# Kernel tuning notes

Hardware: AMD Instinct MI355X
Metric: run time of the kernel (lower is better)

Reference implementation:

```python
import jax, jax.numpy as jnp
import numpy as np

EPS = 1e-8
TAU = 0.2
IOU_THR = 0.5
NEG = -1e9
N, C, H, D_FG, D_CLS = 8192, 1024, 256, 64, 128


def setup_inputs() -> dict:
    key = jax.random.key(0)
    ks = jax.random.split(key, 11)
    def lin(k, fan_in, fan_out):
        return jax.random.normal(k, (fan_in, fan_out), jnp.float32) / np.sqrt(fan_in)
    return {
        "roi_feats": jax.random.normal(ks[0], (N, C), jnp.float32),
        "labels": jax.random.randint(ks[1], (N,), 0, 21, jnp.int32).astype(jnp.int64),
        "ious": jax.random.uniform(ks[2], (N,), jnp.float32),
        "fg_w1": lin(ks[3], C, H), "fg_b1": jnp.zeros((H,), jnp.float32),
        "fg_w2": lin(ks[4], H, D_FG), "fg_b2": jnp.zeros((D_FG,), jnp.float32),
        "cls_w1": lin(ks[5], C, H), "cls_b1": jnp.zeros((H,), jnp.float32),
        "cls_w2": lin(ks[6], H, D_CLS), "cls_b2": jnp.zeros((D_CLS,), jnp.float32),
    }


def _project_normalize(x, w1, b1, w2, b2):
    h = jax.nn.relu(x @ w1 + b1)
    z = h @ w2 + b2
    norm = jnp.maximum(jnp.linalg.norm(z, axis=1, keepdims=True), EPS)
    return z / norm


def _forward(roi_feats, labels, ious, fg_w1, fg_b1, fg_w2, fg_b2, cls_w1, cls_b1, cls_w2, cls_b2):
    n = roi_feats.shape[0]
    z_fg = _project_normalize(roi_feats, fg_w1, fg_b1, fg_w2, fg_b2)
    z_cls = _project_normalize(roi_feats, cls_w1, cls_b1, cls_w2, cls_b2)

    ignore = labels == -1
    fg = (labels > 0) & ~ignore
    iou_weight = jnp.where(ious > IOU_THR, ious, 0.0)
    eye = jnp.eye(n, dtype=bool)

    # ---- fg/bg contrastive (bg_as_negatives_only=True) ----
    sim_fg = (z_fg @ z_fg.T) / TAU                       # [N,N]
    exp_sim = jnp.exp(sim_fg)
    denom = jnp.sum(exp_sim * (~eye).astype(jnp.float32), axis=1)
    pos = (fg & ~ignore)[None, :] & ~eye                 # positives: fg columns, no self
    n_pos = jnp.sum(pos, axis=1)
    numer = jnp.sum(exp_sim * pos.astype(jnp.float32), axis=1)
    # original computes den = denom + EPS then -log((numer+EPS)/(den+EPS))
    loss_i = -jnp.log((numer + EPS) / (denom + 2.0 * EPS))
    valid = (fg & ~ignore) & (n_pos > 0)
    w = iou_weight * valid.astype(jnp.float32)
    loss_fg_bg = jnp.sum(w * loss_i) / (jnp.sum(w) + EPS)

    # ---- class supervised contrastive ----
    sim_cls = (z_cls @ z_cls.T) / TAU
    sim_masked = jnp.where(eye, NEG, sim_cls)
    log_denom = jax.nn.logsumexp(sim_masked, axis=1)     # [N]
    log_p = jnp.where(eye, NEG, sim_cls - log_denom[:, None])
    # pos_mask keeps diagonal (as in original): same label, col not ignore, col label != 0
    posc = (labels[None, :] == labels[:, None]) & (~ignore)[None, :] & (labels[None, :] != 0)
    n_posc = jnp.sum(posc, axis=1).astype(jnp.float32)
    sum_log_p = jnp.sum(log_p * posc.astype(jnp.float32), axis=1)
    valid_c = (fg & ~ignore) & (n_posc > 0) & jnp.isfinite(log_denom)
    Lzi = jnp.where(valid_c, -sum_log_p / (n_posc + EPS), 0.0)
    wc = iou_weight * valid_c.astype(jnp.float32)
    loss_supcon = jnp.sum(wc * Lzi) / (jnp.sum(wc) + EPS)

    return jnp.stack([loss_fg_bg, loss_supcon])


def reference(roi_feats, labels, ious, fg_w1, fg_b1, fg_w2, fg_b2, cls_w1, cls_b1, cls_w2, cls_b2):
    return _forward(roi_feats, labels, ious, fg_w1, fg_b1, fg_w2, fg_b2, cls_w1, cls_b1, cls_w2, cls_b2)
```

## Files before the change

### kernel.cpp

```cpp
#include <hip/hip_runtime.h>


typedef __attribute__((ext_vector_type(8))) short bs8;
typedef __attribute__((ext_vector_type(4))) float f4;

#define MFMA_BF16(a, b, c) __builtin_amdgcn_mfma_f32_16x16x32_bf16((a), (b), (c), 0, 0, 0)

#if defined(__has_builtin)
#if __has_builtin(__builtin_amdgcn_exp2f)
#define EXP2F(x) __builtin_amdgcn_exp2f(x)
#endif
#endif
#ifndef EXP2F
#define EXP2F(x) exp2f(x)
#endif

#define K_LOG2E 7.2134752044448170f

__device__ __forceinline__ unsigned short f2bf(float f) {
  unsigned int u = __float_as_uint(f);
  u = (u + 0x7fffu + ((u >> 16) & 1u)) >> 16;
  return (unsigned short)u;
}
__device__ __forceinline__ float bf2f(unsigned short s) {
  return __uint_as_float(((unsigned int)s) << 16);
}

constexpr size_t O_W1T  = 0;
constexpr size_t O_W2TF = 1048576;
constexpr size_t O_W2TC = 1081344;
constexpr size_t O_H    = 1146880;
constexpr size_t O_ZF   = 9535488;
constexpr size_t O_ZC   = 10584064;
constexpr size_t O_SCLS = 12681216;
constexpr size_t O_ROWD = 12697600;
constexpr size_t O_ROWN = 12730368;
constexpr size_t O_ROWS = 12763136;
constexpr size_t O_SCAL = 12795904;
constexpr size_t O_HIST = 12795920;
constexpr size_t O_NFG  = 12796048;
constexpr int ZERO_WORDS = (int)((O_NFG + 4 - O_SCLS) / 4);

__global__ void __launch_bounds__(256) zero_kernel(float* __restrict__ p, int n) {
  int i = blockIdx.x * 256 + threadIdx.x;
  if (i < n) p[i] = 0.f;
}

__global__ void __launch_bounds__(256) transp_kernel(
    const float* __restrict__ fgw1, const float* __restrict__ clsw1,
    const float* __restrict__ fgw2, const float* __restrict__ clsw2,
    unsigned short* __restrict__ W1T, unsigned short* __restrict__ W2Tf,
    unsigned short* __restrict__ W2Tc) {
  __shared__ float tile[64][65];
  const int m = blockIdx.y;
  const float* src;
  unsigned short* dst;
  int R, C;
  if (m == 0)      { src = fgw1;  dst = W1T;              R = 1024; C = 256; }
  else if (m == 1) { src = clsw1; dst = W1T + 256 * 1024; R = 1024; C = 256; }
  else if (m == 2) { src = fgw2;  dst = W2Tf;             R = 256;  C = 64;  }
  else             { src = clsw2; dst = W2Tc;             R = 256;  C = 128; }
  const int cT = C >> 6;
  if (blockIdx.x >= (R >> 6) * cT) return;
  const int r0 = (blockIdx.x / cT) << 6, c0 = (blockIdx.x % cT) << 6;
  const int t = threadIdx.x;
  {
    const int rr = t >> 4, cc = (t & 15) << 2;
#pragma unroll
    for (int i = 0; i < 4; i++) {
      float4 v = *(const float4*)(src + (size_t)(r0 + rr + i * 16) * C + c0 + cc);
      tile[rr + i * 16][cc] = v.x; tile[rr + i * 16][cc + 1] = v.y;
      tile[rr + i * 16][cc + 2] = v.z; tile[rr + i * 16][cc + 3] = v.w;
    }
  }
  __syncthreads();
  {
    const int dr = t >> 2, dc = (t & 3) << 4;
    bs8 o0, o1;
#pragma unroll
    for (int j = 0; j < 8; j++) o0[j] = (short)f2bf(tile[dc + j][dr]);
#pragma unroll
    for (int j = 0; j < 8; j++) o1[j] = (short)f2bf(tile[dc + 8 + j][dr]);
    unsigned short* dp = dst + (size_t)(c0 + dr) * R + r0 + dc;
    *(bs8*)dp = o0;
    *(bs8*)(dp + 8) = o1;
  }
}

__global__ void __launch_bounds__(256) meta_kernel(const int* __restrict__ labels,
                                                   int* __restrict__ hist,
                                                   int* __restrict__ nfg) {
  __shared__ int sh[33];
  const int t = threadIdx.x;
  if (t < 33) sh[t] = 0;
  __syncthreads();
  int lab = labels[blockIdx.x * 256 + t];
  if (lab >= 0 && lab < 32) atomicAdd(&sh[lab], 1);
  if (lab > 0) atomicAdd(&sh[32], 1);
  __syncthreads();
  if (t < 32 && sh[t] > 0) atomicAdd(&hist[t], sh[t]);
  if (t == 32 && sh[32] > 0) atomicAdd(nfg, sh[32]);
}

__global__ void __launch_bounds__(256) gemm1_kernel(
    const float* __restrict__ X, const unsigned short* __restrict__ W1T,
    const float* __restrict__ b1f, const float* __restrict__ b1c,
    unsigned short* __restrict__ H) {
  __shared__ __align__(16) unsigned short lA[128 * 40];
  __shared__ __align__(16) unsigned short lB[64 * 40];
  const int t = threadIdx.x;
  const int w = t >> 6, lane = t & 63, ln = lane & 15, quad = lane >> 4;
  const int m0 = blockIdx.x * 128, n0 = blockIdx.y * 64;

  f4 acc[2][4];
#pragma unroll
  for (int rs = 0; rs < 2; rs++)
#pragma unroll
    for (int s = 0; s < 4; s++) acc[rs][s] = (f4){0.f, 0.f, 0.f, 0.f};

  for (int k0 = 0; k0 < 1024; k0 += 32) {
    __syncthreads();
#pragma unroll
    for (int i = 0; i < 2; i++) {
      int ch = t + i * 256;
      int r = ch >> 2, c = (ch & 3) * 8;
      const float* xp = X + (size_t)(m0 + r) * 1024 + k0 + c;
      float4 x0 = *(const float4*)xp;
      float4 x1 = *(const float4*)(xp + 4);
      bs8 av;
      av[0] = (short)f2bf(x0.x); av[1] = (short)f2bf(x0.y);
      av[2] = (short)f2bf(x0.z); av[3] = (short)f2bf(x0.w);
      av[4] = (short)f2bf(x1.x); av[5] = (short)f2bf(x1.y);
      av[6] = (short)f2bf(x1.z); av[7] = (short)f2bf(x1.w);
      *(bs8*)&lA[r * 40 + c] = av;
    }
    {
      int r = t >> 2, c = (t & 3) * 8;
      *(bs8*)&lB[r * 40 + c] = *(const bs8*)(W1T + (size_t)(n0 + r) * 1024 + k0 + c);
    }
    __syncthreads();
    bs8 af0 = *(const bs8*)&lA[(w * 32 + ln) * 40 + quad * 8];
    bs8 af1 = *(const bs8*)&lA[(w * 32 + 16 + ln) * 40 + quad * 8];
#pragma unroll
    for (int s = 0; s < 4; s++) {
      bs8 bf = *(const bs8*)&lB[(s * 16 + ln) * 40 + quad * 8];
      acc[0][s] = MFMA_BF16(af0, bf, acc[0][s]);
      acc[1][s] = MFMA_BF16(af1, bf, acc[1][s]);
    }
  }
#pragma unroll
  for (int s = 0; s < 4; s++) {
    int n = n0 + s * 16 + ln;
    float b = (n < 256) ? b1f[n] : b1c[n - 256];
#pragma unroll
    for (int rs = 0; rs < 2; rs++)
#pragma unroll
      for (int r = 0; r < 4; r++) {
        float v = fmaxf(acc[rs][s][r] + b, 0.f);
        H[(size_t)(m0 + w * 32 + rs * 16 + quad * 4 + r) * 512 + n] = f2bf(v);
      }
  }
}

__global__ void __launch_bounds__(256) gemm2_kernel(
    const unsigned short* __restrict__ H,
    const unsigned short* __restrict__ W2Tf, const unsigned short* __restrict__ W2Tc,
    const float* __restrict__ b2f, const float* __restrict__ b2c,
    unsigned short* __restrict__ Zf, unsigned short* __restrict__ Zc) {
  const int t = threadIdx.x;
  const int w = t >> 6, lane = t & 63, ln = lane & 15, quad = lane >> 4;
  const int rw = blockIdx.x * 32 + (w & 1) * 16;

  if (w < 2) {
    const unsigned short* hrow = H + (size_t)(rw + ln) * 512;
    f4 acc[4];
#pragma unroll
    for (int s = 0; s < 4; s++) acc[s] = (f4){0.f, 0.f, 0.f, 0.f};
#pragma unroll
    for (int ks = 0; ks < 8; ks++) {
      bs8 af = *(const bs8*)(hrow + ks * 32 + quad * 8);
#pragma unroll
      for (int s = 0; s < 4; s++) {
        bs8 bf = *(const bs8*)(W2Tf + (size_t)(s * 16 + ln) * 256 + ks * 32 + quad * 8);
        acc[s] = MFMA_BF16(af, bf, acc[s]);
      }
    }
    float ss[4] = {0.f, 0.f, 0.f, 0.f};
#pragma unroll
    for (int s = 0; s < 4; s++) {
      float b = b2f[s * 16 + ln];
#pragma unroll
      for (int r = 0; r < 4; r++) {
        acc[s][r] += b;
        ss[r] = fmaf(acc[s][r], acc[s][r], ss[r]);
      }
    }
#pragma unroll
    for (int r = 0; r < 4; r++) {
#pragma unroll
      for (int off = 1; off < 16; off <<= 1) ss[r] += __shfl_xor(ss[r], off, 64);
      float sc = 1.f / fmaxf(sqrtf(ss[r]), 1e-8f);
#pragma unroll
      for (int s = 0; s < 4; s++)
        Zf[(size_t)(rw + quad * 4 + r) * 64 + s * 16 + ln] = f2bf(acc[s][r] * sc);
    }
  } else {
    const unsigned short* hrow = H + (size_t)(rw + ln) * 512 + 256;
    f4 acc[8];
#pragma unroll
    for (int s = 0; s < 8; s++) acc[s] = (f4){0.f, 0.f, 0.f, 0.f};
#pragma unroll
    for (int ks = 0; ks < 8; ks++) {
      bs8 af = *(const bs8*)(hrow + ks * 32 + quad * 8);
#pragma unroll
      for (int s = 0; s < 8; s++) {
        bs8 bf = *(const bs8*)(W2Tc + (size_t)(s * 16 + ln) * 256 + ks * 32 + quad * 8);
        acc[s] = MFMA_BF16(af, bf, acc[s]);
      }
    }
    float ss[4] = {0.f, 0.f, 0.f, 0.f};
#pragma unroll
    for (int s = 0; s < 8; s++) {
      float b = b2c[s * 16 + ln];
#pragma unroll
      for (int r = 0; r < 4; r++) {
        acc[s][r] += b;
        ss[r] = fmaf(acc[s][r], acc[s][r], ss[r]);
      }
    }
#pragma unroll
    for (int r = 0; r < 4; r++) {
#pragma unroll
      for (int off = 1; off < 16; off <<= 1) ss[r] += __shfl_xor(ss[r], off, 64);
      float sc = 1.f / fmaxf(sqrtf(ss[r]), 1e-8f);
#pragma unroll
      for (int s = 0; s < 8; s++)
        Zc[(size_t)(rw + quad * 4 + r) * 128 + s * 16 + ln] = f2bf(acc[s][r] * sc);
    }
  }
}

__global__ void __launch_bounds__(128) scls_kernel(const unsigned short* __restrict__ Zc,
                                                   const int* __restrict__ labels,
                                                   float* __restrict__ Scls) {
  const int c = blockIdx.x + 1;
  const int t = threadIdx.x;
  const int r0 = blockIdx.y * 256;
  float acc = 0.f;
#pragma unroll 4
  for (int r = r0; r < r0 + 256; r++) {
    if (labels[r] == c) acc += bf2f(Zc[(size_t)r * 128 + t]);
  }
  atomicAdd(&Scls[c * 128 + t], acc);
}

__global__ void __launch_bounds__(256) sim_kernel(
    const unsigned short* __restrict__ Zf, const unsigned short* __restrict__ Zc,
    const int* __restrict__ labels,
    float* __restrict__ rowD, float* __restrict__ rowN, float* __restrict__ rowS) {
  __shared__ __align__(16) unsigned short sZf[64 * 72];
  __shared__ __align__(16) unsigned short sZc[64 * 136];
  __shared__ float sFg[64];
  const int t = threadIdx.x;
  const int w = t >> 6, lane = t & 63, ln = lane & 15, quad = lane >> 4;
  const int rbase = blockIdx.x * 128 + w * 32;

  bs8 afg[2][2], acl[2][4];
#pragma unroll
  for (int rs = 0; rs < 2; rs++) {
    const unsigned short* zf = Zf + (size_t)(rbase + rs * 16 + ln) * 64;
    const unsigned short* zc = Zc + (size_t)(rbase + rs * 16 + ln) * 128;
#pragma unroll
    for (int s = 0; s < 2; s++) afg[rs][s] = *(const bs8*)(zf + s * 32 + quad * 8);
#pragma unroll
    for (int s = 0; s < 4; s++) acl[rs][s] = *(const bs8*)(zc + s * 32 + quad * 8);
  }

  float dacc[2][4] = {}, nacc[2][4] = {}, sacc[2][4] = {};

  for (int ct = 0; ct < 8; ct++) {
    const int c0 = blockIdx.y * 512 + ct * 64;
    __syncthreads();
#pragma unroll
    for (int i = 0; i < 2; i++) {
      int ch = t + i * 256;
      int j = ch >> 3, c8 = (ch & 7) * 8;
      *(bs8*)&sZf[j * 72 + c8] = *(const bs8*)(Zf + (size_t)(c0 + j) * 64 + c8);
    }
#pragma unroll
    for (int i = 0; i < 4; i++) {
      int ch = t + i * 256;
      int j = ch >> 4, c8 = (ch & 15) * 8;
      *(bs8*)&sZc[j * 136 + c8] = *(const bs8*)(Zc + (size_t)(c0 + j) * 128 + c8);
    }
    if (t < 64) sFg[t] = (labels[c0 + t] > 0) ? 1.f : 0.f;
    __syncthreads();

#pragma unroll
    for (int s = 0; s < 4; s++) {
      const int lcol = s * 16 + ln;
      const float fgc = sFg[lcol];
      bs8 b0 = *(const bs8*)&sZf[lcol * 72 + quad * 8];
      bs8 b1 = *(const bs8*)&sZf[lcol * 72 + 32 + quad * 8];
#pragma unroll
      for (int rs = 0; rs < 2; rs++) {
        f4 c = {0.f, 0.f, 0.f, 0.f};
        c = MFMA_BF16(afg[rs][0], b0, c);
        c = MFMA_BF16(afg[rs][1], b1, c);
#pragma unroll
        for (int r = 0; r < 4; r++) {
          float e = EXP2F(c[r] * K_LOG2E);
          dacc[rs][r] += e;
          nacc[rs][r] = fmaf(fgc, e, nacc[rs][r]);
        }
      }
      bs8 bc0 = *(const bs8*)&sZc[lcol * 136 + quad * 8];
      bs8 bc1 = *(const bs8*)&sZc[lcol * 136 + 32 + quad * 8];
      bs8 bc2 = *(const bs8*)&sZc[lcol * 136 + 64 + quad * 8];
      bs8 bc3 = *(const bs8*)&sZc[lcol * 136 + 96 + quad * 8];
#pragma unroll
      for (int rs = 0; rs < 2; rs++) {
        f4 c = {0.f, 0.f, 0.f, 0.f};
        c = MFMA_BF16(acl[rs][0], bc0, c);
        c = MFMA_BF16(acl[rs][1], bc1, c);
        c = MFMA_BF16(acl[rs][2], bc2, c);
        c = MFMA_BF16(acl[rs][3], bc3, c);
#pragma unroll
        for (int r = 0; r < 4; r++) sacc[rs][r] += EXP2F(c[r] * K_LOG2E);
      }
    }
  }

#pragma unroll
  for (int rs = 0; rs < 2; rs++)
#pragma unroll
    for (int r = 0; r < 4; r++) {
      float d = dacc[rs][r], n = nacc[rs][r], s = sacc[rs][r];
#pragma unroll
      for (int off = 1; off < 16; off <<= 1) {
        d += __shfl_xor(d, off, 64);
        n += __shfl_xor(n, off, 64);
        s += __shfl_xor(s, off, 64);
      }
      if (ln == 0) {
        int row = rbase + rs * 16 + quad * 4 + r;
        atomicAdd(&rowD[row], d);
        atomicAdd(&rowN[row], n);
        atomicAdd(&rowS[row], s);
      }
    }
}

__global__ void __launch_bounds__(256) finalize_kernel(
    const unsigned short* __restrict__ Zf, const unsigned short* __restrict__ Zc,
    const int* __restrict__ labels, const float* __restrict__ ious,
    const float* __restrict__ rowD, const float* __restrict__ rowN,
    const float* __restrict__ rowS, const float* __restrict__ Scls,
    const int* __restrict__ hist, const int* __restrict__ nfg,
    float* __restrict__ scal) {
  __shared__ float red[4][4];
  const int t = threadIdx.x, w = t >> 6, lane = t & 63;
  float aw0 = 0.f, al0 = 0.f, aw1 = 0.f, al1 = 0.f;
  const int NFG = *nfg;
  for (int it = 0; it < 16; it++) {
    const int i = it * 512 + blockIdx.x * 4 + w;
    const int lab = labels[i];
    if (lab > 0 && lab < 32) {
      const float iou = ious[i];
      const float iw = (iou > 0.5f) ? iou : 0.f;
      float dot = 0.f, ssq = 0.f;
#pragma unroll
      for (int p = 0; p < 2; p++) {
        const int k = lane + p * 64;
        const float z = bf2f(Zc[(size_t)i * 128 + k]);
        dot = fmaf(z, Scls[lab * 128 + k], dot);
        ssq = fmaf(z, z, ssq);
      }
      float zf = bf2f(Zf[(size_t)i * 64 + lane]);
      float ssqf = zf * zf;
#pragma unroll
      for (int off = 1; off < 64; off <<= 1) {
        dot += __shfl_xor(dot, off, 64);
        ssq += __shfl_xor(ssq, off, 64);
        ssqf += __shfl_xor(ssqf, off, 64);
      }
      if (lane == 0) {
        const float ef = EXP2F(K_LOG2E * ssqf);
        if (NFG - 1 > 0) {
          const float D = rowD[i] - ef;
          const float Nn = rowN[i] - ef;
          const float loss = logf(D + 2e-8f) - logf(Nn + 1e-8f);
          aw0 += iw;
          al0 += iw * loss;
        }
        const int npc = hist[lab];
        if (npc > 0) {
          const float S = rowS[i] - EXP2F(K_LOG2E * ssq);
          const float logden = logf(S);
          const float slp = (dot - ssq) * 5.0f - (float)(npc - 1) * logden - 1e9f;
          aw1 += iw;
          al1 += iw * (-slp / ((float)npc + 1e-8f));
        }
      }
    }
  }
  if (lane == 0) { red[w][0] = aw0; red[w][1] = al0; red[w][2] = aw1; red[w][3] = al1; }
  __syncthreads();
  if (t < 4) atomicAdd(&scal[t], red[0][t] + red[1][t] + red[2][t] + red[3][t]);
}

__global__ void writeout_kernel(const float* __restrict__ scal, float* __restrict__ out) {
  if (threadIdx.x == 0) {
    out[0] = scal[1] / (scal[0] + 1e-8f);
    out[1] = scal[3] / (scal[2] + 1e-8f);
  }
}

extern "C" void kernel_launch(void* const* d_in, const int* in_sizes, int n_in,
                              void* d_out, int out_size, void* d_ws, size_t ws_size,
                              hipStream_t stream) {
  (void)in_sizes; (void)n_in; (void)out_size; (void)ws_size;
  const float* roi    = (const float*)d_in[0];
  const int*   labels = (const int*)d_in[1];
  const float* ious   = (const float*)d_in[2];
  const float* fgw1   = (const float*)d_in[3];
  const float* fgb1   = (const float*)d_in[4];
  const float* fgw2   = (const float*)d_in[5];
  const float* fgb2   = (const float*)d_in[6];
  const float* clsw1  = (const float*)d_in[7];
  const float* clsb1  = (const float*)d_in[8];
  const float* clsw2  = (const float*)d_in[9];
  const float* clsb2  = (const float*)d_in[10];

  char* ws = (char*)d_ws;
  unsigned short* W1T  = (unsigned short*)(ws + O_W1T);
  unsigned short* W2Tf = (unsigned short*)(ws + O_W2TF);
  unsigned short* W2Tc = (unsigned short*)(ws + O_W2TC);
  unsigned short* Hb   = (unsigned short*)(ws + O_H);
  unsigned short* Zf   = (unsigned short*)(ws + O_ZF);
  unsigned short* Zc   = (unsigned short*)(ws + O_ZC);
  float* Scls = (float*)(ws + O_SCLS);
  float* rowD = (float*)(ws + O_ROWD);
  float* rowN = (float*)(ws + O_ROWN);
  float* rowS = (float*)(ws + O_ROWS);
  float* scal = (float*)(ws + O_SCAL);
  int* hist = (int*)(ws + O_HIST);
  int* nfg  = (int*)(ws + O_NFG);
  float* out = (float*)d_out;

  hipLaunchKernelGGL(zero_kernel, dim3((ZERO_WORDS + 255) / 256), dim3(256), 0, stream,
                     (float*)(ws + O_SCLS), ZERO_WORDS);
  hipLaunchKernelGGL(transp_kernel, dim3(64, 4), dim3(256), 0, stream,
                     fgw1, clsw1, fgw2, clsw2, W1T, W2Tf, W2Tc);
  hipLaunchKernelGGL(meta_kernel, dim3(32), dim3(256), 0, stream, labels, hist, nfg);
  hipLaunchKernelGGL(gemm1_kernel, dim3(64, 8), dim3(256), 0, stream,
                     roi, W1T, fgb1, clsb1, Hb);
  hipLaunchKernelGGL(gemm2_kernel, dim3(256), dim3(256), 0, stream,
                     Hb, W2Tf, W2Tc, fgb2, clsb2, Zf, Zc);
  hipLaunchKernelGGL(scls_kernel, dim3(20, 32), dim3(128), 0, stream, Zc, labels, Scls);
  hipLaunchKernelGGL(sim_kernel, dim3(64, 16), dim3(256), 0, stream,
                     Zf, Zc, labels, rowD, rowN, rowS);
  hipLaunchKernelGGL(finalize_kernel, dim3(128), dim3(256), 0, stream,
                     Zf, Zc, labels, ious, rowD, rowN, rowS, Scls, hist, nfg, scal);
  hipLaunchKernelGGL(writeout_kernel, dim3(1), dim3(64), 0, stream, scal, out);
}
```

Baseline: 220.5 us.

## Exploit similarity symmetry by computing only upper-triangle tiles in sim kernel

Each sim_kernel block now processes one 128x128 tile pair (bi, bi+d) from the upper triangle of the symmetric similarity matrix. It accumulates row sums as before and also column sums, which are reduced across waves through shared memory and atomically added to the column rows' accumulators. This roughly halves the MFMA and exp work of the N×N similarity pass. In exchange it adds column-side accumulators and register pressure, an extra shared-memory reduction and more atomics, and some blocks in the d=32 slice exit early.

```diff
diff --git a/kernel.cpp b/kernel.cpp
--- a/kernel.cpp
+++ b/kernel.cpp
@@ -258,14 +258,21 @@
     const unsigned short* __restrict__ Zf, const unsigned short* __restrict__ Zc,
     const int* __restrict__ labels,
     float* __restrict__ rowD, float* __restrict__ rowN, float* __restrict__ rowS) {
+  const int bi = blockIdx.x, d = blockIdx.y;
+  if (d == 32 && bi >= 32) return;
+  const int bj = (bi + d) & 63;
+  const bool diag = (d == 0);
+
   __shared__ __align__(16) unsigned short sZf[64 * 72];
   __shared__ __align__(16) unsigned short sZc[64 * 136];
   __shared__ float sFg[64];
+  __shared__ float sCol[4][2][4][16][3];
   const int t = threadIdx.x;
   const int w = t >> 6, lane = t & 63, ln = lane & 15, quad = lane >> 4;
-  const int rbase = blockIdx.x * 128 + w * 32;
+  const int rbase = bi * 128 + w * 32;
 
   bs8 afg[2][2], acl[2][4];
+  float fgr[2][4];
 #pragma unroll
   for (int rs = 0; rs < 2; rs++) {
     const unsigned short* zf = Zf + (size_t)(rbase + rs * 16 + ln) * 64;
@@ -274,12 +281,17 @@
     for (int s = 0; s < 2; s++) afg[rs][s] = *(const bs8*)(zf + s * 32 + quad * 8);
 #pragma unroll
     for (int s = 0; s < 4; s++) acl[rs][s] = *(const bs8*)(zc + s * 32 + quad * 8);
+#pragma unroll
+    for (int r = 0; r < 4; r++)
+      fgr[rs][r] = (labels[rbase + rs * 16 + quad * 4 + r] > 0) ? 1.f : 0.f;
   }
 
   float dacc[2][4] = {}, nacc[2][4] = {}, sacc[2][4] = {};
-
-  for (int ct = 0; ct < 8; ct++) {
-    const int c0 = blockIdx.y * 512 + ct * 64;
+  float cdacc[2][4] = {}, cnacc[2][4] = {}, csacc[2][4] = {};
+
+#pragma unroll
+  for (int ct = 0; ct < 2; ct++) {
+    const int c0 = bj * 128 + ct * 64;
     __syncthreads();
 #pragma unroll
     for (int i = 0; i < 2; i++) {
@@ -312,6 +324,8 @@
           float e = EXP2F(c[r] * K_LOG2E);
           dacc[rs][r] += e;
           nacc[rs][r] = fmaf(fgc, e, nacc[rs][r]);
+          cdacc[ct][s] += e;
+          cnacc[ct][s] = fmaf(fgr[rs][r], e, cnacc[ct][s]);
         }
       }
       bs8 bc0 = *(const bs8*)&sZc[lcol * 136 + quad * 8];
@@ -326,7 +340,11 @@
         c = MFMA_BF16(acl[rs][2], bc2, c);
         c = MFMA_BF16(acl[rs][3], bc3, c);
 #pragma unroll
-        for (int r = 0; r < 4; r++) sacc[rs][r] += EXP2F(c[r] * K_LOG2E);
+        for (int r = 0; r < 4; r++) {
+          float e = EXP2F(c[r] * K_LOG2E);
+          sacc[rs][r] += e;
+          csacc[ct][s] += e;
+        }
       }
     }
   }
@@ -335,20 +353,55 @@
   for (int rs = 0; rs < 2; rs++)
 #pragma unroll
     for (int r = 0; r < 4; r++) {
-      float d = dacc[rs][r], n = nacc[rs][r], s = sacc[rs][r];
+      float dv = dacc[rs][r], nv = nacc[rs][r], sv = sacc[rs][r];
 #pragma unroll
       for (int off = 1; off < 16; off <<= 1) {
-        d += __shfl_xor(d, off, 64);
-        n += __shfl_xor(n, off, 64);
-        s += __shfl_xor(s, off, 64);
+        dv += __shfl_xor(dv, off, 64);
+        nv += __shfl_xor(nv, off, 64);
+        sv += __shfl_xor(sv, off, 64);
       }
       if (ln == 0) {
         int row = rbase + rs * 16 + quad * 4 + r;
-        atomicAdd(&rowD[row], d);
-        atomicAdd(&rowN[row], n);
-        atomicAdd(&rowS[row], s);
-      }
-    }
+        atomicAdd(&rowD[row], dv);
+        atomicAdd(&rowN[row], nv);
+        atomicAdd(&rowS[row], sv);
+      }
+    }
+
+  if (!diag) {
+#pragma unroll
+    for (int ct = 0; ct < 2; ct++)
+#pragma unroll
+      for (int s = 0; s < 4; s++) {
+        float dv = cdacc[ct][s], nv = cnacc[ct][s], sv = csacc[ct][s];
+#pragma unroll
+        for (int off = 16; off < 64; off <<= 1) {
+          dv += __shfl_xor(dv, off, 64);
+          nv += __shfl_xor(nv, off, 64);
+          sv += __shfl_xor(sv, off, 64);
+        }
+        if (quad == 0) {
+          sCol[w][ct][s][ln][0] = dv;
+          sCol[w][ct][s][ln][1] = nv;
+          sCol[w][ct][s][ln][2] = sv;
+        }
+      }
+    __syncthreads();
+    if (t < 128) {
+      const int ct = t >> 6, s = (t >> 4) & 3, lm = t & 15;
+      float dv = 0.f, nv = 0.f, sv = 0.f;
+#pragma unroll
+      for (int ww = 0; ww < 4; ww++) {
+        dv += sCol[ww][ct][s][lm][0];
+        nv += sCol[ww][ct][s][lm][1];
+        sv += sCol[ww][ct][s][lm][2];
+      }
+      const int col = bj * 128 + t;
+      atomicAdd(&rowD[col], dv);
+      atomicAdd(&rowN[col], nv);
+      atomicAdd(&rowS[col], sv);
+    }
+  }
 }
 
 __global__ void __launch_bounds__(256) finalize_kernel(
@@ -458,7 +511,7 @@
   hipLaunchKernelGGL(gemm2_kernel, dim3(256), dim3(256), 0, stream,
                      Hb, W2Tf, W2Tc, fgb2, clsb2, Zf, Zc);
   hipLaunchKernelGGL(scls_kernel, dim3(20, 32), dim3(128), 0, stream, Zc, labels, Scls);
-  hipLaunchKernelGGL(sim_kernel, dim3(64, 16), dim3(256), 0, stream,
+  hipLaunchKernelGGL(sim_kernel, dim3(64, 33), dim3(256), 0, stream,
                      Zf, Zc, labels, rowD, rowN, rowS);
   hipLaunchKernelGGL(finalize_kernel, dim3(128), dim3(256), 0, stream,
                      Zf, Zc, labels, ious, rowD, rowN, rowS, Scls, hist, nfg, scal);
```

Measured after the change: 221.9 us. Within noise of the previous version (+0.6%).
